# Performance work log

Hardware: AMD Instinct MI355X
Metric: run time of the kernel (lower is better)

## Reference

```python
import jax, jax.numpy as jnp
import numpy as np

B, T, D, H = 2, 2048, 768, 12
HD = D // H  # head_dim = 64


def setup_inputs() -> dict:
    key = jax.random.key(0)
    ks = jax.random.split(key, 10)
    s = 0.02
    return {
        "hidden_states": jax.random.normal(ks[0], (B, T, D), jnp.float32),
        "attention_mask": jnp.zeros((B, 1, T, T), jnp.float32),
        "relative_position_bias": jax.random.normal(ks[1], (H, T, T), jnp.float32) * s,
        "Wq": jax.random.normal(ks[2], (D, D), jnp.float32) * s,
        "bq": jnp.zeros((D,), jnp.float32),
        "Wk": jax.random.normal(ks[3], (D, D), jnp.float32) * s,
        "bk": jnp.zeros((D,), jnp.float32),
        "Wv": jax.random.normal(ks[4], (D, D), jnp.float32) * s,
        "bv": jnp.zeros((D,), jnp.float32),
        "Wo": jax.random.normal(ks[5], (D, D), jnp.float32) * s,
        "bo": jnp.zeros((D,), jnp.float32),
    }


def reference(hidden_states, attention_mask, relative_position_bias,
              Wq, bq, Wk, bk, Wv, bv, Wo, bo):
    b, t, d = hidden_states.shape
    scale = HD ** -0.5
    # projections (nn.Linear: x @ W^T + b)
    q = (hidden_states @ Wq.T + bq) * scale
    k = hidden_states @ Wk.T + bk
    v = hidden_states @ Wv.T + bv
    # [b, h, t, hd]
    q = q.reshape(b, t, H, HD).transpose(0, 2, 1, 3)
    k = k.reshape(b, t, H, HD).transpose(0, 2, 1, 3)
    v = v.reshape(b, t, H, HD).transpose(0, 2, 1, 3)
    # scores: [b, h, t, s]
    attn = jnp.einsum("bhtd,bhsd->bhts", q, k)
    attn = attn + relative_position_bias[None, :, :, :]
    attn = attn + attention_mask  # (b,1,t,s) broadcast over heads
    attn = jax.nn.softmax(attn, axis=-1)
    out = jnp.einsum("bhts,bhsd->bhtd", attn, v)
    out = out.transpose(0, 2, 1, 3).reshape(b, t, d)
    return out @ Wo.T + bo
```

## Files before the change

### kernel.cpp

```cpp
#include <hip/hip_runtime.h>

#define B_  2
#define T_  2048
#define D_  768
#define H_  12
#define HD_ 64

typedef short bf16x8 __attribute__((ext_vector_type(8)));
typedef float f32x4  __attribute__((ext_vector_type(4)));
typedef unsigned int u32;

static __device__ __forceinline__ unsigned short f2bf(float f) {
    union { float f; unsigned u; } v; v.f = f;
    unsigned r = (v.u + 0x7FFFu + ((v.u >> 16) & 1u)) >> 16;
    return (unsigned short)r;
}

__global__ void cvt_f32_bf16(const float* __restrict__ in,
                             unsigned short* __restrict__ out, int n8) {
    int i = blockIdx.x * blockDim.x + threadIdx.x;
    int stride = gridDim.x * blockDim.x;
    for (; i < n8; i += stride) {
        float4 a = *(const float4*)(in + (size_t)i * 8);
        float4 b = *(const float4*)(in + (size_t)i * 8 + 4);
        union { unsigned short s[8]; int4 v; } o;
        o.s[0] = f2bf(a.x); o.s[1] = f2bf(a.y); o.s[2] = f2bf(a.z); o.s[3] = f2bf(a.w);
        o.s[4] = f2bf(b.x); o.s[5] = f2bf(b.y); o.s[6] = f2bf(b.z); o.s[7] = f2bf(b.w);
        *(int4*)(out + (size_t)i * 8) = o.v;
    }
}

__global__ void cvt_weights(const float* __restrict__ w0, const float* __restrict__ w1,
                            const float* __restrict__ w2, const float* __restrict__ w3,
                            unsigned short* __restrict__ out, int n8) {
    const float* src = (blockIdx.y == 0) ? w0 : (blockIdx.y == 1) ? w1
                     : (blockIdx.y == 2) ? w2 : w3;
    unsigned short* dst = out + (size_t)blockIdx.y * (D_ * D_);
    int i = blockIdx.x * blockDim.x + threadIdx.x;
    int stride = gridDim.x * blockDim.x;
    for (; i < n8; i += stride) {
        float4 a = *(const float4*)(src + (size_t)i * 8);
        float4 b = *(const float4*)(src + (size_t)i * 8 + 4);
        union { unsigned short s[8]; int4 v; } o;
        o.s[0] = f2bf(a.x); o.s[1] = f2bf(a.y); o.s[2] = f2bf(a.z); o.s[3] = f2bf(a.w);
        o.s[4] = f2bf(b.x); o.s[5] = f2bf(b.y); o.s[6] = f2bf(b.z); o.s[7] = f2bf(b.w);
        *(int4*)(dst + (size_t)i * 8) = o.v;
    }
}

__global__ __launch_bounds__(256)
void gemm_bt_lds(const unsigned short* __restrict__ A,
                 const unsigned short* __restrict__ W,
                 const float* __restrict__ b0, const float* __restrict__ b1,
                 const float* __restrict__ b2,
                 void* __restrict__ outp, int mode)
{
    __shared__ __align__(16) unsigned short As[128 * 32];
    __shared__ __align__(16) unsigned short Bs[64 * 32];

    const int tid  = threadIdx.x;
    const int lane = tid & 63;
    const int wid  = tid >> 6;
    const int wm   = wid >> 1, wn = wid & 1;
    const int l15  = lane & 15, l16 = lane >> 4;
    const int bm   = blockIdx.x * 128, bn = blockIdx.y * 64;

    f32x4 acc[4][2];
    #pragma unroll
    for (int mi = 0; mi < 4; ++mi)
        #pragma unroll
        for (int ni = 0; ni < 2; ++ni)
            acc[mi][ni] = (f32x4){0.f, 0.f, 0.f, 0.f};

    const int srow = lane >> 2;
    const int scol = (lane & 3) * 8;

    for (int k0 = 0; k0 < 768; k0 += 32) {
        #pragma unroll
        for (int j = 0; j < 3; ++j) {
            int c = wid * 3 + j;
            const unsigned short* src;
            unsigned short* dst;
            if (c < 8) {
                src = A + (size_t)(bm + c * 16 + srow) * 768 + k0 + scol;
                dst = As + c * 512;
            } else {
                src = W + (size_t)(bn + (c - 8) * 16 + srow) * 768 + k0 + scol;
                dst = Bs + (c - 8) * 512;
            }
            __builtin_amdgcn_global_load_lds(
                (const __attribute__((address_space(1))) u32*)src,
                (__attribute__((address_space(3))) u32*)dst, 16, 0, 0);
        }
        __syncthreads();

        bf16x8 af[4], bfr[2];
        #pragma unroll
        for (int mi = 0; mi < 4; ++mi)
            af[mi] = *(const bf16x8*)(As + (wm * 64 + mi * 16 + l15) * 32 + l16 * 8);
        #pragma unroll
        for (int ni = 0; ni < 2; ++ni)
            bfr[ni] = *(const bf16x8*)(Bs + (wn * 32 + ni * 16 + l15) * 32 + l16 * 8);
        #pragma unroll
        for (int mi = 0; mi < 4; ++mi)
            #pragma unroll
            for (int ni = 0; ni < 2; ++ni)
                acc[mi][ni] = __builtin_amdgcn_mfma_f32_16x16x32_bf16(
                    af[mi], bfr[ni], acc[mi][ni], 0, 0, 0);
        __syncthreads();
    }

    if (mode == 1) {
        const int sel = bn / 768;
        const float* bp = (sel == 0) ? b0 : (sel == 1) ? b1 : b2;
        const float scale = (sel == 0) ? 0.125f : 1.0f;
        unsigned short* o = (unsigned short*)outp + (size_t)sel * (B_ * T_ * D_);
        #pragma unroll
        for (int ni = 0; ni < 2; ++ni) {
            int cg = bn - sel * 768 + wn * 32 + ni * 16 + l15;
            float bv = bp[cg];
            int h = cg >> 6, hd = cg & 63;
            #pragma unroll
            for (int mi = 0; mi < 4; ++mi)
                #pragma unroll
                for (int reg = 0; reg < 4; ++reg) {
                    int row = bm + wm * 64 + mi * 16 + l16 * 4 + reg;
                    int bb = row >> 11, t = row & (T_ - 1);
                    float v = (acc[mi][ni][reg] + bv) * scale;
                    o[(((size_t)bb * H_ + h) * T_ + t) * HD_ + hd] = f2bf(v);
                }
        }
    } else {
        float* o = (float*)outp;
        #pragma unroll
        for (int ni = 0; ni < 2; ++ni) {
            int col = bn + wn * 32 + ni * 16 + l15;
            float bv = b0[col];
            #pragma unroll
            for (int mi = 0; mi < 4; ++mi)
                #pragma unroll
                for (int reg = 0; reg < 4; ++reg) {
                    int row = bm + wm * 64 + mi * 16 + l16 * 4 + reg;
                    o[(size_t)row * 768 + col] = acc[mi][ni][reg] + bv;
                }
        }
    }
}

__global__ __launch_bounds__(256)
void attn_fwd_mfma(const unsigned short* __restrict__ q,
                   const unsigned short* __restrict__ k,
                   const unsigned short* __restrict__ v,
                   const float* __restrict__ bias,
                   const float* __restrict__ mask,
                   unsigned short* __restrict__ ctx)
{
    __shared__ __align__(16) unsigned short Ks[64 * 72];
    __shared__ __align__(16) unsigned short Vt[64 * 72];
    __shared__ __align__(16) unsigned short Ps[64 * 72];

    const int tid  = threadIdx.x;
    const int lane = tid & 63;
    const int wq   = tid >> 6;
    const int l15  = lane & 15, l16 = lane >> 4;
    const int bh   = blockIdx.y;
    const int b    = bh / H_, h = bh % H_;
    const int q0   = blockIdx.x * 64;

    const unsigned short* qb = q + (size_t)bh * T_ * HD_;
    const unsigned short* kb = k + (size_t)bh * T_ * HD_;
    const unsigned short* vb = v + (size_t)bh * T_ * HD_;

    bf16x8 qf[2];
    {
        const unsigned short* qp = qb + (size_t)(q0 + wq * 16 + l15) * HD_;
        qf[0] = *(const bf16x8*)(qp + l16 * 8);
        qf[1] = *(const bf16x8*)(qp + 32 + l16 * 8);
    }

    float m_run = -3.0e38f, l_run = 0.f;
    f32x4 o[4];
    #pragma unroll
    for (int f = 0; f < 4; ++f) o[f] = (f32x4){0.f, 0.f, 0.f, 0.f};

    const size_t brow = (size_t)h * T_ * T_ + (size_t)(q0 + wq * 16 + l15) * T_;
    const size_t mrow = (size_t)b * T_ * T_ + (size_t)(q0 + wq * 16 + l15) * T_;

    for (int s0 = 0; s0 < T_; s0 += 64) {
        #pragma unroll
        for (int it = 0; it < 2; ++it) {
            int slot = tid + it * 256;
            int row = slot >> 3, c8 = (slot & 7) * 8;
            int4 kv = *(const int4*)(kb + (size_t)(s0 + row) * HD_ + c8);
            *(int4*)(Ks + row * 72 + c8) = kv;
            int key = slot & 63, hd0 = (slot >> 6) * 8;
            int4 vv = *(const int4*)(vb + (size_t)(s0 + key) * HD_ + hd0);
            const unsigned short* vs = (const unsigned short*)&vv;
            #pragma unroll
            for (int e = 0; e < 8; ++e)
                Vt[(hd0 + e) * 72 + key] = vs[e];
        }

        float4 bv4[4], mv4[4];
        #pragma unroll
        for (int f = 0; f < 4; ++f) {
            bv4[f] = *(const float4*)(bias + brow + s0 + f * 16 + l16 * 4);
            mv4[f] = *(const float4*)(mask + mrow + s0 + f * 16 + l16 * 4);
        }
        __syncthreads();

        f32x4 s[4];
        #pragma unroll
        for (int f = 0; f < 4; ++f) {
            bf16x8 k0f = *(const bf16x8*)(Ks + (f * 16 + l15) * 72 + l16 * 8);
            bf16x8 k1f = *(const bf16x8*)(Ks + (f * 16 + l15) * 72 + 32 + l16 * 8);
            f32x4 t = (f32x4){0.f, 0.f, 0.f, 0.f};
            t = __builtin_amdgcn_mfma_f32_16x16x32_bf16(k0f, qf[0], t, 0, 0, 0);
            t = __builtin_amdgcn_mfma_f32_16x16x32_bf16(k1f, qf[1], t, 0, 0, 0);
            s[f] = t;
        }

        #pragma unroll
        for (int f = 0; f < 4; ++f) {
            const float* pb = (const float*)&bv4[f];
            const float* pm = (const float*)&mv4[f];
            #pragma unroll
            for (int reg = 0; reg < 4; ++reg)
                s[f][reg] += pb[reg] + pm[reg];
        }

        float mx = s[0][0];
        #pragma unroll
        for (int f = 0; f < 4; ++f)
            #pragma unroll
            for (int reg = 0; reg < 4; ++reg)
                mx = fmaxf(mx, s[f][reg]);
        mx = fmaxf(mx, __shfl_xor(mx, 16));
        mx = fmaxf(mx, __shfl_xor(mx, 32));
        float m_new = fmaxf(m_run, mx);
        float scv = __expf(m_run - m_new);
        float psum = 0.f;
        #pragma unroll
        for (int f = 0; f < 4; ++f)
            #pragma unroll
            for (int reg = 0; reg < 4; ++reg) {
                float p = __expf(s[f][reg] - m_new);
                s[f][reg] = p; psum += p;
            }
        psum += __shfl_xor(psum, 16);
        psum += __shfl_xor(psum, 32);
        l_run = l_run * scv + psum;
        m_run = m_new;

        float scq[4];
        #pragma unroll
        for (int reg = 0; reg < 4; ++reg) scq[reg] = __shfl(scv, l16 * 4 + reg);
        #pragma unroll
        for (int f = 0; f < 4; ++f)
            #pragma unroll
            for (int reg = 0; reg < 4; ++reg)
                o[f][reg] *= scq[reg];

        unsigned short* Pw = Ps + wq * 16 * 72;
        #pragma unroll
        for (int f = 0; f < 4; ++f) {
            ushort4 pk;
            pk.x = f2bf(s[f][0]); pk.y = f2bf(s[f][1]);
            pk.z = f2bf(s[f][2]); pk.w = f2bf(s[f][3]);
            *(ushort4*)(Pw + l15 * 72 + f * 16 + l16 * 4) = pk;
        }

        #pragma unroll
        for (int kc = 0; kc < 2; ++kc) {
            bf16x8 pf = *(const bf16x8*)(Pw + l15 * 72 + kc * 32 + l16 * 8);
            #pragma unroll
            for (int f = 0; f < 4; ++f) {
                bf16x8 vf = *(const bf16x8*)(Vt + (f * 16 + l15) * 72 + kc * 32 + l16 * 8);
                o[f] = __builtin_amdgcn_mfma_f32_16x16x32_bf16(pf, vf, o[f], 0, 0, 0);
            }
        }
        __syncthreads();
    }

    float linv[4];
    #pragma unroll
    for (int reg = 0; reg < 4; ++reg)
        linv[reg] = 1.0f / __shfl(l_run, l16 * 4 + reg);
    #pragma unroll
    for (int reg = 0; reg < 4; ++reg) {
        int t = q0 + wq * 16 + l16 * 4 + reg;
        unsigned short* cb = ctx + ((size_t)b * T_ + t) * D_ + h * HD_;
        #pragma unroll
        for (int f = 0; f < 4; ++f)
            cb[f * 16 + l15] = f2bf(o[f][reg] * linv[reg]);
    }
}

extern "C" void kernel_launch(void* const* d_in, const int* in_sizes, int n_in,
                              void* d_out, int out_size, void* d_ws, size_t ws_size,
                              hipStream_t stream) {
    const float* hs   = (const float*)d_in[0];
    const float* mask = (const float*)d_in[1];
    const float* bias = (const float*)d_in[2];
    const float* Wq   = (const float*)d_in[3];
    const float* bq   = (const float*)d_in[4];
    const float* Wk   = (const float*)d_in[5];
    const float* bk   = (const float*)d_in[6];
    const float* Wv   = (const float*)d_in[7];
    const float* bv   = (const float*)d_in[8];
    const float* Wo   = (const float*)d_in[9];
    const float* bo   = (const float*)d_in[10];
    float* out = (float*)d_out;

    const size_t NE = (size_t)B_ * T_ * D_;
    const size_t WE = (size_t)D_ * D_;
    unsigned short* ws = (unsigned short*)d_ws;
    unsigned short* hs_bf = ws;
    unsigned short* wbf   = hs_bf + NE;
    unsigned short* qkv   = wbf + 4 * WE;
    unsigned short* ctxb  = qkv + 3 * NE;

    cvt_f32_bf16<<<dim3(1536), 256, 0, stream>>>(hs, hs_bf, (int)(NE / 8));
    cvt_weights<<<dim3(288, 4), 256, 0, stream>>>(Wq, Wk, Wv, Wo, wbf, (int)(WE / 8));

    gemm_bt_lds<<<dim3(32, 36), 256, 0, stream>>>(hs_bf, wbf, bq, bk, bv, qkv, 1);

    attn_fwd_mfma<<<dim3(T_ / 64, B_ * H_), 256, 0, stream>>>(
        qkv, qkv + NE, qkv + 2 * NE, bias, mask, ctxb);

    gemm_bt_lds<<<dim3(32, 12), 256, 0, stream>>>(ctxb, wbf + 3 * WE, bo, nullptr, nullptr, out, 0);
}
```

Before: 477.0 us.

## Split attention key range across two wave groups, enlarge GEMM tiles, lazy rescale

The attention kernel now runs 512 threads, with two groups of four waves each covering half the key sequence (split-K). The partial softmax states are merged through shared memory at the end. K is read directly from global memory instead of being staged in LDS. V is double-buffered with register prefetch, and bias and mask are prefetched one tile ahead. The online softmax skips rescaling unless the running max grows by more than 8. Separately, the GEMM tile grows to 128x128 with a 4x4 accumulator per wave. These changes aim to raise parallelism and overlap loads with compute, at the cost of more register pressure, an extra block-wide sync per iteration, and fewer GEMM blocks.

```diff
diff --git a/kernel.cpp b/kernel.cpp
--- a/kernel.cpp
+++ b/kernel.cpp
@@ -56,20 +56,20 @@
                  void* __restrict__ outp, int mode)
 {
     __shared__ __align__(16) unsigned short As[128 * 32];
-    __shared__ __align__(16) unsigned short Bs[64 * 32];
+    __shared__ __align__(16) unsigned short Bs[128 * 32];
 
     const int tid  = threadIdx.x;
     const int lane = tid & 63;
     const int wid  = tid >> 6;
     const int wm   = wid >> 1, wn = wid & 1;
     const int l15  = lane & 15, l16 = lane >> 4;
-    const int bm   = blockIdx.x * 128, bn = blockIdx.y * 64;
-
-    f32x4 acc[4][2];
+    const int bm   = blockIdx.x * 128, bn = blockIdx.y * 128;
+
+    f32x4 acc[4][4];
     #pragma unroll
     for (int mi = 0; mi < 4; ++mi)
         #pragma unroll
-        for (int ni = 0; ni < 2; ++ni)
+        for (int ni = 0; ni < 4; ++ni)
             acc[mi][ni] = (f32x4){0.f, 0.f, 0.f, 0.f};
 
     const int srow = lane >> 2;
@@ -77,8 +77,8 @@
 
     for (int k0 = 0; k0 < 768; k0 += 32) {
         #pragma unroll
-        for (int j = 0; j < 3; ++j) {
-            int c = wid * 3 + j;
+        for (int j = 0; j < 4; ++j) {
+            int c = wid * 4 + j;
             const unsigned short* src;
             unsigned short* dst;
             if (c < 8) {
@@ -94,17 +94,17 @@
         }
         __syncthreads();
 
-        bf16x8 af[4], bfr[2];
+        bf16x8 af[4], bfr[4];
         #pragma unroll
         for (int mi = 0; mi < 4; ++mi)
             af[mi] = *(const bf16x8*)(As + (wm * 64 + mi * 16 + l15) * 32 + l16 * 8);
         #pragma unroll
-        for (int ni = 0; ni < 2; ++ni)
-            bfr[ni] = *(const bf16x8*)(Bs + (wn * 32 + ni * 16 + l15) * 32 + l16 * 8);
+        for (int ni = 0; ni < 4; ++ni)
+            bfr[ni] = *(const bf16x8*)(Bs + (wn * 64 + ni * 16 + l15) * 32 + l16 * 8);
         #pragma unroll
         for (int mi = 0; mi < 4; ++mi)
             #pragma unroll
-            for (int ni = 0; ni < 2; ++ni)
+            for (int ni = 0; ni < 4; ++ni)
                 acc[mi][ni] = __builtin_amdgcn_mfma_f32_16x16x32_bf16(
                     af[mi], bfr[ni], acc[mi][ni], 0, 0, 0);
         __syncthreads();
@@ -116,8 +116,8 @@
         const float scale = (sel == 0) ? 0.125f : 1.0f;
         unsigned short* o = (unsigned short*)outp + (size_t)sel * (B_ * T_ * D_);
         #pragma unroll
-        for (int ni = 0; ni < 2; ++ni) {
-            int cg = bn - sel * 768 + wn * 32 + ni * 16 + l15;
+        for (int ni = 0; ni < 4; ++ni) {
+            int cg = bn - sel * 768 + wn * 64 + ni * 16 + l15;
             float bv = bp[cg];
             int h = cg >> 6, hd = cg & 63;
             #pragma unroll
@@ -133,8 +133,8 @@
     } else {
         float* o = (float*)outp;
         #pragma unroll
-        for (int ni = 0; ni < 2; ++ni) {
-            int col = bn + wn * 32 + ni * 16 + l15;
+        for (int ni = 0; ni < 4; ++ni) {
+            int col = bn + wn * 64 + ni * 16 + l15;
             float bv = b0[col];
             #pragma unroll
             for (int mi = 0; mi < 4; ++mi)
@@ -147,7 +147,7 @@
     }
 }
 
-__global__ __launch_bounds__(256)
+__global__ __launch_bounds__(512, 4)
 void attn_fwd_mfma(const unsigned short* __restrict__ q,
                    const unsigned short* __restrict__ k,
                    const unsigned short* __restrict__ v,
@@ -155,13 +155,18 @@
                    const float* __restrict__ mask,
                    unsigned short* __restrict__ ctx)
 {
-    __shared__ __align__(16) unsigned short Ks[64 * 72];
-    __shared__ __align__(16) unsigned short Vt[64 * 72];
-    __shared__ __align__(16) unsigned short Ps[64 * 72];
+    __shared__ __align__(16) unsigned char Lraw[52224];
+    unsigned short* VtBuf = (unsigned short*)Lraw;
+    unsigned short* PsBuf = (unsigned short*)(Lraw + 34816);
+    float* Osh = (float*)Lraw;
+    float* Msh = (float*)(Lraw + 16640);
+    float* Lsh = (float*)(Lraw + 16896);
 
     const int tid  = threadIdx.x;
     const int lane = tid & 63;
-    const int wq   = tid >> 6;
+    const int wid  = tid >> 6;
+    const int g    = wid >> 2;
+    const int wq   = wid & 3;
     const int l15  = lane & 15, l16 = lane >> 4;
     const int bh   = blockIdx.y;
     const int b    = bh / H_, h = bh % H_;
@@ -170,6 +175,10 @@
     const unsigned short* qb = q + (size_t)bh * T_ * HD_;
     const unsigned short* kb = k + (size_t)bh * T_ * HD_;
     const unsigned short* vb = v + (size_t)bh * T_ * HD_;
+
+    unsigned short* Vt0 = VtBuf + (g * 2 + 0) * 4352;
+    unsigned short* Vt1 = VtBuf + (g * 2 + 1) * 4352;
+    unsigned short* Pw  = PsBuf + wid * 1088;
 
     bf16x8 qf[2];
     {
@@ -186,34 +195,41 @@
     const size_t brow = (size_t)h * T_ * T_ + (size_t)(q0 + wq * 16 + l15) * T_;
     const size_t mrow = (size_t)b * T_ * T_ + (size_t)(q0 + wq * 16 + l15) * T_;
 
-    for (int s0 = 0; s0 < T_; s0 += 64) {
-        #pragma unroll
-        for (int it = 0; it < 2; ++it) {
-            int slot = tid + it * 256;
-            int row = slot >> 3, c8 = (slot & 7) * 8;
-            int4 kv = *(const int4*)(kb + (size_t)(s0 + row) * HD_ + c8);
-            *(int4*)(Ks + row * 72 + c8) = kv;
-            int key = slot & 63, hd0 = (slot >> 6) * 8;
-            int4 vv = *(const int4*)(vb + (size_t)(s0 + key) * HD_ + hd0);
-            const unsigned short* vs = (const unsigned short*)&vv;
-            #pragma unroll
-            for (int e = 0; e < 8; ++e)
-                Vt[(hd0 + e) * 72 + key] = vs[e];
-        }
-
-        float4 bv4[4], mv4[4];
+    const int tg   = tid & 255;
+    const int vkey = tg & 63, vhd0 = (tg >> 6) * 8;
+
+    int s0 = g * 1024;
+    int4 vr0 = *(const int4*)(vb + (size_t)(s0 + vkey) * HD_ + vhd0);
+    int4 vr1 = *(const int4*)(vb + (size_t)(s0 + vkey) * HD_ + vhd0 + 32);
+    float4 bv4[4], mv4[4];
+    #pragma unroll
+    for (int f = 0; f < 4; ++f) {
+        bv4[f] = *(const float4*)(bias + brow + s0 + f * 16 + l16 * 4);
+        mv4[f] = *(const float4*)(mask + mrow + s0 + f * 16 + l16 * 4);
+    }
+
+    for (int i = 0; i < 16; ++i, s0 += 64) {
+        unsigned short* Vtc = (i & 1) ? Vt1 : Vt0;
+        {
+            const unsigned short* a = (const unsigned short*)&vr0;
+            const unsigned short* c = (const unsigned short*)&vr1;
+            #pragma unroll
+            for (int e = 0; e < 8; ++e) {
+                Vtc[(vhd0 + e) * 68 + vkey]      = a[e];
+                Vtc[(vhd0 + 32 + e) * 68 + vkey] = c[e];
+            }
+        }
+        if (i < 15) {
+            vr0 = *(const int4*)(vb + (size_t)(s0 + 64 + vkey) * HD_ + vhd0);
+            vr1 = *(const int4*)(vb + (size_t)(s0 + 64 + vkey) * HD_ + vhd0 + 32);
+        }
+        __syncthreads();
+
+        f32x4 s[4];
         #pragma unroll
         for (int f = 0; f < 4; ++f) {
-            bv4[f] = *(const float4*)(bias + brow + s0 + f * 16 + l16 * 4);
-            mv4[f] = *(const float4*)(mask + mrow + s0 + f * 16 + l16 * 4);
-        }
-        __syncthreads();
-
-        f32x4 s[4];
-        #pragma unroll
-        for (int f = 0; f < 4; ++f) {
-            bf16x8 k0f = *(const bf16x8*)(Ks + (f * 16 + l15) * 72 + l16 * 8);
-            bf16x8 k1f = *(const bf16x8*)(Ks + (f * 16 + l15) * 72 + 32 + l16 * 8);
+            bf16x8 k0f = *(const bf16x8*)(kb + (size_t)(s0 + f * 16 + l15) * HD_ + l16 * 8);
+            bf16x8 k1f = *(const bf16x8*)(kb + (size_t)(s0 + f * 16 + l15) * HD_ + 32 + l16 * 8);
             f32x4 t = (f32x4){0.f, 0.f, 0.f, 0.f};
             t = __builtin_amdgcn_mfma_f32_16x16x32_bf16(k0f, qf[0], t, 0, 0, 0);
             t = __builtin_amdgcn_mfma_f32_16x16x32_bf16(k1f, qf[1], t, 0, 0, 0);
@@ -228,6 +244,13 @@
             for (int reg = 0; reg < 4; ++reg)
                 s[f][reg] += pb[reg] + pm[reg];
         }
+        if (i < 15) {
+            #pragma unroll
+            for (int f = 0; f < 4; ++f) {
+                bv4[f] = *(const float4*)(bias + brow + s0 + 64 + f * 16 + l16 * 4);
+                mv4[f] = *(const float4*)(mask + mrow + s0 + 64 + f * 16 + l16 * 4);
+            }
+        }
 
         float mx = s[0][0];
         #pragma unroll
@@ -237,62 +260,85 @@
                 mx = fmaxf(mx, s[f][reg]);
         mx = fmaxf(mx, __shfl_xor(mx, 16));
         mx = fmaxf(mx, __shfl_xor(mx, 32));
-        float m_new = fmaxf(m_run, mx);
-        float scv = __expf(m_run - m_new);
+        if (!__all(mx - m_run <= 8.f)) {
+            float m_new = fmaxf(m_run, mx);
+            float scv = __expf(m_run - m_new);
+            l_run *= scv;
+            m_run = m_new;
+            float scq[4];
+            #pragma unroll
+            for (int reg = 0; reg < 4; ++reg) scq[reg] = __shfl(scv, l16 * 4 + reg);
+            #pragma unroll
+            for (int f = 0; f < 4; ++f)
+                #pragma unroll
+                for (int reg = 0; reg < 4; ++reg)
+                    o[f][reg] *= scq[reg];
+        }
         float psum = 0.f;
         #pragma unroll
         for (int f = 0; f < 4; ++f)
             #pragma unroll
             for (int reg = 0; reg < 4; ++reg) {
-                float p = __expf(s[f][reg] - m_new);
+                float p = __expf(s[f][reg] - m_run);
                 s[f][reg] = p; psum += p;
             }
         psum += __shfl_xor(psum, 16);
         psum += __shfl_xor(psum, 32);
-        l_run = l_run * scv + psum;
-        m_run = m_new;
-
-        float scq[4];
-        #pragma unroll
-        for (int reg = 0; reg < 4; ++reg) scq[reg] = __shfl(scv, l16 * 4 + reg);
-        #pragma unroll
-        for (int f = 0; f < 4; ++f)
-            #pragma unroll
-            for (int reg = 0; reg < 4; ++reg)
-                o[f][reg] *= scq[reg];
-
-        unsigned short* Pw = Ps + wq * 16 * 72;
+        l_run += psum;
+
         #pragma unroll
         for (int f = 0; f < 4; ++f) {
             ushort4 pk;
             pk.x = f2bf(s[f][0]); pk.y = f2bf(s[f][1]);
             pk.z = f2bf(s[f][2]); pk.w = f2bf(s[f][3]);
-            *(ushort4*)(Pw + l15 * 72 + f * 16 + l16 * 4) = pk;
-        }
+            *(ushort4*)(Pw + l15 * 68 + f * 16 + l16 * 4) = pk;
+        }
+        __syncthreads();
 
         #pragma unroll
         for (int kc = 0; kc < 2; ++kc) {
-            bf16x8 pf = *(const bf16x8*)(Pw + l15 * 72 + kc * 32 + l16 * 8);
+            bf16x8 pf = *(const bf16x8*)(Pw + l15 * 68 + kc * 32 + l16 * 8);
             #pragma unroll
             for (int f = 0; f < 4; ++f) {
-                bf16x8 vf = *(const bf16x8*)(Vt + (f * 16 + l15) * 72 + kc * 32 + l16 * 8);
+                bf16x8 vf = *(const bf16x8*)(Vtc + (f * 16 + l15) * 68 + kc * 32 + l16 * 8);
                 o[f] = __builtin_amdgcn_mfma_f32_16x16x32_bf16(pf, vf, o[f], 0, 0, 0);
             }
         }
-        __syncthreads();
-    }
-
-    float linv[4];
-    #pragma unroll
-    for (int reg = 0; reg < 4; ++reg)
-        linv[reg] = 1.0f / __shfl(l_run, l16 * 4 + reg);
-    #pragma unroll
-    for (int reg = 0; reg < 4; ++reg) {
-        int t = q0 + wq * 16 + l16 * 4 + reg;
-        unsigned short* cb = ctx + ((size_t)b * T_ + t) * D_ + h * HD_;
-        #pragma unroll
-        for (int f = 0; f < 4; ++f)
-            cb[f * 16 + l15] = f2bf(o[f][reg] * linv[reg]);
+    }
+
+    __syncthreads();
+    if (g == 1) {
+        #pragma unroll
+        for (int reg = 0; reg < 4; ++reg) {
+            int qrow = wq * 16 + l16 * 4 + reg;
+            #pragma unroll
+            for (int f = 0; f < 4; ++f)
+                Osh[qrow * 65 + f * 16 + l15] = o[f][reg];
+        }
+        if (l16 == 0) {
+            Msh[wq * 16 + l15] = m_run;
+            Lsh[wq * 16 + l15] = l_run;
+        }
+    }
+    __syncthreads();
+    if (g == 0) {
+        #pragma unroll
+        for (int reg = 0; reg < 4; ++reg) {
+            int qrow = wq * 16 + l16 * 4 + reg;
+            float m0 = __shfl(m_run, l16 * 4 + reg);
+            float l0 = __shfl(l_run, l16 * 4 + reg);
+            float m1 = Msh[qrow], l1 = Lsh[qrow];
+            float M  = fmaxf(m0, m1);
+            float a0 = __expf(m0 - M), a1 = __expf(m1 - M);
+            float inv = 1.0f / (l0 * a0 + l1 * a1);
+            int t = q0 + qrow;
+            unsigned short* cb = ctx + ((size_t)b * T_ + t) * D_ + h * HD_;
+            #pragma unroll
+            for (int f = 0; f < 4; ++f) {
+                float val = (o[f][reg] * a0 + Osh[qrow * 65 + f * 16 + l15] * a1) * inv;
+                cb[f * 16 + l15] = f2bf(val);
+            }
+        }
     }
 }
 
@@ -323,10 +369,10 @@
     cvt_f32_bf16<<<dim3(1536), 256, 0, stream>>>(hs, hs_bf, (int)(NE / 8));
     cvt_weights<<<dim3(288, 4), 256, 0, stream>>>(Wq, Wk, Wv, Wo, wbf, (int)(WE / 8));
 
-    gemm_bt_lds<<<dim3(32, 36), 256, 0, stream>>>(hs_bf, wbf, bq, bk, bv, qkv, 1);
-
-    attn_fwd_mfma<<<dim3(T_ / 64, B_ * H_), 256, 0, stream>>>(
+    gemm_bt_lds<<<dim3(32, 18), 256, 0, stream>>>(hs_bf, wbf, bq, bk, bv, qkv, 1);
+
+    attn_fwd_mfma<<<dim3(T_ / 64, B_ * H_), 512, 0, stream>>>(
         qkv, qkv + NE, qkv + 2 * NE, bias, mask, ctxb);
 
-    gemm_bt_lds<<<dim3(32, 12), 256, 0, stream>>>(ctxb, wbf + 3 * WE, bo, nullptr, nullptr, out, 0);
-}
+    gemm_bt_lds<<<dim3(32, 6), 256, 0, stream>>>(ctxb, wbf + 3 * WE, bo, nullptr, nullptr, out, 0);
+}
```

After: 594.8 us. 24.7% more time.
